# Kernel optimization log

Hardware: AMD Instinct MI355X
Metric: run time of the kernel (lower is better)

The kernel has to match this reference:

```python
import jax, jax.numpy as jnp
import numpy as np


def log_g(x):
    # log of g(x) = x + 0.5 for x>=0, sigmoid(x) for x<0
    return jnp.where(x >= 0, jnp.log(jax.nn.relu(x) + 0.5), -jax.nn.softplus(-x))


def setup_inputs() -> dict:
    key = jax.random.key(0)
    k1, k2, k3 = jax.random.split(key, 3)
    bs, seq_len, d_in, H = 4, 4096, 1024, 1024
    scale = 1.0 / np.sqrt(d_in)  # keep pre-activations O(1) so exp() in log-space scan stays finite
    x = jax.random.normal(k1, (bs, seq_len, d_in), dtype=jnp.float32)
    h_0 = jnp.zeros((bs, 1, H), dtype=jnp.float32)
    Wz = jax.random.normal(k2, (H, d_in), dtype=jnp.float32) * scale
    bz = jnp.zeros((H,), dtype=jnp.float32)
    Wh = jax.random.normal(k3, (H, d_in), dtype=jnp.float32) * scale
    bh = jnp.zeros((H,), dtype=jnp.float32)
    return {"x": x, "h_0": h_0, "Wz": Wz, "bz": bz, "Wh": Wh, "bh": bh}


def reference(x, h_0, Wz, bz, Wh, bh):
    bs, seq_len, _ = x.shape
    # gate and candidate pre-activations (two GEMMs)
    k = jnp.einsum("bsd,hd->bsh", x, Wz) + bz          # [bs, S, H]
    log_coeff = -jax.nn.softplus(k)                     # log(1 - z)
    log_z = -jax.nn.softplus(-k)                        # log(z)
    log_tilde_h = log_g(jnp.einsum("bsd,hd->bsh", x, Wh) + bh)
    log_h_0 = log_g(h_0)                                # [bs, 1, H]
    log_value = jnp.concatenate([log_h_0, log_z + log_tilde_h], axis=1)  # [bs, S+1, H]
    # log-space parallel scan: h_t = (1-z_t) h_{t-1} + z_t h~_t
    a_star = jnp.pad(jnp.cumsum(log_coeff, axis=1), ((0, 0), (1, 0), (0, 0)))  # [bs, S+1, H]
    log_h0_plus_b_star = jax.lax.cumlogsumexp(log_value - a_star, axis=1)
    log_prefix = a_star + log_h0_plus_b_star
    return jnp.exp(log_prefix)[:, 1:]                   # [bs, S, H]
```

## Files before the change

### kernel.cpp

```cpp
#include <hip/hip_runtime.h>
#include <cstddef>
#include <cstdint>

#define BSZ   4
#define SEQ   4096
#define DIN   1024
#define HDIM  1024
#define MTOT  (BSZ * SEQ)
#define NELE  ((size_t)MTOT * HDIM)
#define NX    ((size_t)MTOT * DIN)
#define NW    ((size_t)HDIM * DIN)
#define NCH   128
#define CL    (SEQ / NCH)

#define BM 128
#define BN 64
#define BK 32

#define X4 (NX / 4)
#define W4 (NW / 4)

using bf16x8 = __attribute__((ext_vector_type(8))) __bf16;
using f32x4  = __attribute__((ext_vector_type(4))) float;

__device__ __forceinline__ float bf2f(unsigned int u16bits) {
    union { unsigned int i; float f; } v;
    v.i = u16bits << 16;
    return v.f;
}
__device__ __forceinline__ unsigned int pk2(float a, float b) {
    union { float f; unsigned int i; } ua, ub; ua.f = a; ub.f = b;
    return ((ua.i + 0x8000u) >> 16) | ((ub.i + 0x8000u) & 0xffff0000u);
}

__device__ __forceinline__ void gload16(const void* g, void* l) {
    __builtin_amdgcn_global_load_lds(
        (const __attribute__((address_space(1))) unsigned int*)g,
        (__attribute__((address_space(3))) unsigned int*)l, 16, 0, 0);
}

__global__ __launch_bounds__(256) void cvt_bf16(
    const float* __restrict__ x, const float* __restrict__ wz,
    const float* __restrict__ wh, unsigned short* __restrict__ xb,
    unsigned short* __restrict__ zb, unsigned short* __restrict__ hb)
{
    const size_t i = (size_t)blockIdx.x * 256 + threadIdx.x;
    const float4* s; uint4* d; size_t off;
    const size_t xh = X4 / 2, wh4 = W4 / 2;
    if (i < xh)            { s = (const float4*)x;  d = (uint4*)xb; off = i; }
    else if (i < xh + wh4) { s = (const float4*)wz; d = (uint4*)zb; off = i - xh; }
    else                   { s = (const float4*)wh; d = (uint4*)hb; off = i - xh - wh4; }
    const float4 v0 = s[2 * off];
    const float4 v1 = s[2 * off + 1];
    uint4 r;
    r.x = pk2(v0.x, v0.y); r.y = pk2(v0.z, v0.w);
    r.z = pk2(v1.x, v1.y); r.w = pk2(v1.z, v1.w);
    d[off] = r;
}

__global__ __launch_bounds__(256, 2) void gemm_act_mfma(
    const unsigned short* __restrict__ xb, const unsigned short* __restrict__ zb,
    const unsigned short* __restrict__ hb, const float* __restrict__ bz,
    const float* __restrict__ bh, unsigned int* __restrict__ ab,
    float* __restrict__ carryA, float* __restrict__ carryB)
{
    __shared__ unsigned short xs[BM * BK];
    __shared__ unsigned short zs[BN * BK];
    __shared__ unsigned short hs[BN * BK];

    const int tid  = threadIdx.x;
    const int wid  = tid >> 6;
    const int lane = tid & 63;
    const int lm   = lane & 15;
    const int q    = lane >> 4;
    const int wy   = wid >> 1;
    const int wx   = wid & 1;

    const int m0 = blockIdx.y * BM;
    const int n0 = blockIdx.x * BN;

    const int slr   = lane >> 2;
    const int sbyte = (lane & 3) << 4;
    const char* gx = (const char*)xb + ((size_t)(m0 + wid * 32 + slr) * DIN) * 2 + sbyte;
    const char* gz = (const char*)zb + ((size_t)(n0 + wid * 16 + slr) * DIN) * 2 + sbyte;
    const char* gh = (const char*)hb + ((size_t)(n0 + wid * 16 + slr) * DIN) * 2 + sbyte;
    char* xl = (char*)xs + wid * 2048;
    char* zl = (char*)zs + wid * 1024;
    char* hl = (char*)hs + wid * 1024;

    f32x4 acc1[4][2], acc2[4][2];
#pragma unroll
    for (int mt = 0; mt < 4; ++mt)
#pragma unroll
        for (int nt = 0; nt < 2; ++nt) {
            acc1[mt][nt] = (f32x4){0.f, 0.f, 0.f, 0.f};
            acc2[mt][nt] = (f32x4){0.f, 0.f, 0.f, 0.f};
        }

    for (int k0 = 0; k0 < DIN; k0 += BK) {
        const size_t kb = (size_t)k0 * 2;
        __syncthreads();
        gload16(gx + kb,          xl);
        gload16(gx + kb + 32768,  xl + 1024);
        gload16(gz + kb,          zl);
        gload16(gh + kb,          hl);
        __syncthreads();

        bf16x8 a[4];
#pragma unroll
        for (int mt = 0; mt < 4; ++mt)
            a[mt] = *(const bf16x8*)((const char*)xs + ((wy * 64 + mt * 16 + lm) * 64 + q * 16));
#pragma unroll
        for (int nt = 0; nt < 2; ++nt) {
            const int bo = (wx * 32 + nt * 16 + lm) * 64 + q * 16;
            const bf16x8 vz = *(const bf16x8*)((const char*)zs + bo);
            const bf16x8 vh = *(const bf16x8*)((const char*)hs + bo);
#pragma unroll
            for (int mt = 0; mt < 4; ++mt) {
                acc1[mt][nt] = __builtin_amdgcn_mfma_f32_16x16x32_bf16(a[mt], vz, acc1[mt][nt], 0, 0, 0);
                acc2[mt][nt] = __builtin_amdgcn_mfma_f32_16x16x32_bf16(a[mt], vh, acc2[mt][nt], 0, 0, 0);
            }
        }
    }

    const int bi    = m0 >> 12;
    const int cbase = ((m0 & 4095) >> 5) + wy * 2;

#pragma unroll
    for (int nt = 0; nt < 2; ++nt) {
        const int col = n0 + wx * 32 + nt * 16 + lm;
        const float bzv = bz[col];
        const float bhv = bh[col];
#pragma unroll
        for (int half = 0; half < 2; ++half) {
            float CA = 1.f, CB = 0.f;
#pragma unroll
            for (int mi = 0; mi < 2; ++mi) {
                const int mt = half * 2 + mi;
                const int row0 = m0 + wy * 64 + mt * 16 + q * 4;
                float A = 1.f, B = 0.f;
#pragma unroll
                for (int r = 0; r < 4; ++r) {
                    const float kpre = acc1[mt][nt][r] + bzv;
                    const float hpre = acc2[mt][nt][r] + bhv;
                    const float ez   = __expf(-kpre);
                    const float zv   = 1.0f / (1.0f + ez);
                    const float av   = ez * zv;
                    const float g    = (hpre >= 0.f) ? (hpre + 0.5f)
                                                     : (1.0f / (1.0f + __expf(-hpre)));
                    const float bv   = zv * g;
                    ab[(size_t)(row0 + r) * HDIM + col] = pk2(av, bv);
                    A = av * A;
                    B = fmaf(av, B, bv);
                }
                float A2 = __shfl_xor(A, 16, 64);
                float B2 = __shfl_xor(B, 16, 64);
                B = (q & 1) ? fmaf(A, B2, B) : fmaf(A2, B, B2);
                A = A * A2;
                A2 = __shfl_xor(A, 32, 64);
                B2 = __shfl_xor(B, 32, 64);
                B = (q & 2) ? fmaf(A, B2, B) : fmaf(A2, B, B2);
                A = A * A2;
                CB = fmaf(A, CB, B);
                CA = A * CA;
            }
            if (q == 0) {
                const int cseq = cbase + half;
                const size_t ci = ((size_t)(cseq * BSZ + bi)) * HDIM + col;
                carryA[ci] = CA;
                carryB[ci] = CB;
            }
        }
    }
}

__global__ __launch_bounds__(256) void scan_phaseB(
    const float* __restrict__ h0, const float* __restrict__ carryA,
    const float* __restrict__ carryB, float* __restrict__ hin)
{
    const int h  = blockIdx.x * 256 + threadIdx.x;
    const int bi = blockIdx.y;
    const float v = h0[(size_t)bi * HDIM + h];
    float hr = (v >= 0.0f) ? (v + 0.5f) : (1.0f / (1.0f + __expf(-v)));
    for (int c = 0; c < NCH; ++c) {
        const size_t ci = ((size_t)c * BSZ + bi) * HDIM + h;
        hin[ci] = hr;
        hr = fmaf(carryA[ci], hr, carryB[ci]);
    }
}

__global__ __launch_bounds__(256) void scan_phaseC(
    const unsigned int* __restrict__ ab, const float* __restrict__ hin,
    float* __restrict__ out)
{
    const int c  = blockIdx.x;
    const int bi = blockIdx.y;
    const int h  = threadIdx.x * 4;
    size_t idx = ((size_t)bi * SEQ + (size_t)c * CL) * HDIM + h;
    const size_t ci = ((size_t)c * BSZ + bi) * HDIM + h;
    float4 hr = *(const float4*)&hin[ci];
#pragma unroll 4
    for (int t = 0; t < CL; ++t) {
        const uint4 v = *(const uint4*)&ab[idx];
        hr.x = fmaf(bf2f(v.x & 0xffffu), hr.x, bf2f(v.x >> 16));
        hr.y = fmaf(bf2f(v.y & 0xffffu), hr.y, bf2f(v.y >> 16));
        hr.z = fmaf(bf2f(v.z & 0xffffu), hr.z, bf2f(v.z >> 16));
        hr.w = fmaf(bf2f(v.w & 0xffffu), hr.w, bf2f(v.w >> 16));
        *(float4*)&out[idx] = hr;
        idx += HDIM;
    }
}

extern "C" void kernel_launch(void* const* d_in, const int* in_sizes, int n_in,
                              void* d_out, int out_size, void* d_ws, size_t ws_size,
                              hipStream_t stream)
{
    const float* x  = (const float*)d_in[0];
    const float* h0 = (const float*)d_in[1];
    const float* Wz = (const float*)d_in[2];
    const float* bz = (const float*)d_in[3];
    const float* Wh = (const float*)d_in[4];
    const float* bh = (const float*)d_in[5];
    float* out = (float*)d_out;

    unsigned int*   ab  = (unsigned int*)d_ws;
    unsigned short* xbf = (unsigned short*)(ab + NELE);
    unsigned short* zbf = xbf + NX;
    unsigned short* hbf = zbf + NW;
    float* carryA = (float*)(hbf + NW);
    float* carryB = carryA + (size_t)NCH * BSZ * HDIM;
    float* hin    = carryB + (size_t)NCH * BSZ * HDIM;

    const int cvtBlocks = (int)((X4 + 2 * W4) / 2 / 256);
    cvt_bf16<<<cvtBlocks, 256, 0, stream>>>(x, Wz, Wh, xbf, zbf, hbf);

    dim3 gGrid(HDIM / BN, MTOT / BM);
    gemm_act_mfma<<<gGrid, 256, 0, stream>>>(xbf, zbf, hbf, bz, bh, ab, carryA, carryB);

    dim3 bGrid(HDIM / 256, BSZ);
    scan_phaseB<<<bGrid, 256, 0, stream>>>(h0, carryA, carryB, hin);

    dim3 cGrid(NCH, BSZ);
    scan_phaseC<<<cGrid, 256, 0, stream>>>(ab, hin, out);
}
```

Measured before the change: 253.0 us.

## Rewrite fused dual GEMM as double-buffered 256x128 tile with phased MFMA schedule

Replaces the 128x64x32 single-buffered GEMM with a 512-thread kernel using 256x128x64 tiles and double-buffered LDS. Global-to-LDS prefetch of the next K tile is split across phases that alternate with MFMA bursts, using setprio and explicit waitcnt. It also adds an XOR swizzle on LDS to avoid bank conflicts and a grid swizzle for L2 locality. The aim is to hide load latency and raise MFMA utilisation. In exchange it uses many more accumulator registers and 128 KB of LDS per block, which may limit occupancy.

```diff
diff --git a/kernel.cpp b/kernel.cpp
--- a/kernel.cpp
+++ b/kernel.cpp
@@ -13,12 +13,13 @@
 #define NCH   128
 #define CL    (SEQ / NCH)
 
-#define BM 128
-#define BN 64
-#define BK 32
-
 #define X4 (NX / 4)
 #define W4 (NW / 4)
+
+#define GBM 256
+#define GBN 128
+#define GBK 64
+#define NKT (DIN / GBK)
 
 using bf16x8 = __attribute__((ext_vector_type(8))) __bf16;
 using f32x4  = __attribute__((ext_vector_type(4))) float;
@@ -58,100 +59,175 @@
     d[off] = r;
 }
 
-__global__ __launch_bounds__(256, 2) void gemm_act_mfma(
+#define MFMA16(p)                                                              \
+    _Pragma("unroll")                                                          \
+    for (int i_ = 0; i_ < 2; ++i_) {                                           \
+        _Pragma("unroll")                                                      \
+        for (int nt_ = 0; nt_ < 2; ++nt_) {                                    \
+            accz[2*(p)+i_][nt_] = __builtin_amdgcn_mfma_f32_16x16x32_bf16(     \
+                av[i_][0], fz[nt_][0], accz[2*(p)+i_][nt_], 0, 0, 0);          \
+            acch[2*(p)+i_][nt_] = __builtin_amdgcn_mfma_f32_16x16x32_bf16(     \
+                av[i_][0], fh[nt_][0], acch[2*(p)+i_][nt_], 0, 0, 0);          \
+            accz[2*(p)+i_][nt_] = __builtin_amdgcn_mfma_f32_16x16x32_bf16(     \
+                av[i_][1], fz[nt_][1], accz[2*(p)+i_][nt_], 0, 0, 0);          \
+            acch[2*(p)+i_][nt_] = __builtin_amdgcn_mfma_f32_16x16x32_bf16(     \
+                av[i_][1], fh[nt_][1], acch[2*(p)+i_][nt_], 0, 0, 0);          \
+        }                                                                      \
+    }
+
+#define PHASE(p, STAGE)                                                        \
+    {                                                                          \
+        bf16x8 av[2][2];                                                       \
+        _Pragma("unroll")                                                      \
+        for (int i_ = 0; i_ < 2; ++i_) {                                       \
+            av[i_][0] = *(const bf16x8*)(bcc + aBase + (2*(p)+i_) * 2048 + k0o);\
+            av[i_][1] = *(const bf16x8*)(bcc + aBase + (2*(p)+i_) * 2048 + k1o);\
+        }                                                                      \
+        STAGE                                                                  \
+        __builtin_amdgcn_s_barrier();                                          \
+        asm volatile("s_waitcnt lgkmcnt(0)" ::: "memory");                     \
+        __builtin_amdgcn_sched_barrier(0);                                     \
+        __builtin_amdgcn_s_setprio(1);                                         \
+        MFMA16(p)                                                              \
+        __builtin_amdgcn_s_setprio(0);                                         \
+        __builtin_amdgcn_s_barrier();                                          \
+    }
+
+__global__ __launch_bounds__(512, 2) void gemm_act_8ph(
     const unsigned short* __restrict__ xb, const unsigned short* __restrict__ zb,
     const unsigned short* __restrict__ hb, const float* __restrict__ bz,
     const float* __restrict__ bh, unsigned int* __restrict__ ab,
     float* __restrict__ carryA, float* __restrict__ carryB)
 {
-    __shared__ unsigned short xs[BM * BK];
-    __shared__ unsigned short zs[BN * BK];
-    __shared__ unsigned short hs[BN * BK];
+    __shared__ unsigned short smem[2][32768];
 
     const int tid  = threadIdx.x;
     const int wid  = tid >> 6;
     const int lane = tid & 63;
     const int lm   = lane & 15;
     const int q    = lane >> 4;
-    const int wy   = wid >> 1;
-    const int wx   = wid & 1;
-
-    const int m0 = blockIdx.y * BM;
-    const int n0 = blockIdx.x * BN;
-
-    const int slr   = lane >> 2;
-    const int sbyte = (lane & 3) << 4;
-    const char* gx = (const char*)xb + ((size_t)(m0 + wid * 32 + slr) * DIN) * 2 + sbyte;
-    const char* gz = (const char*)zb + ((size_t)(n0 + wid * 16 + slr) * DIN) * 2 + sbyte;
-    const char* gh = (const char*)hb + ((size_t)(n0 + wid * 16 + slr) * DIN) * 2 + sbyte;
-    char* xl = (char*)xs + wid * 2048;
-    char* zl = (char*)zs + wid * 1024;
-    char* hl = (char*)hs + wid * 1024;
-
-    f32x4 acc1[4][2], acc2[4][2];
-#pragma unroll
-    for (int mt = 0; mt < 4; ++mt)
+    const int wr   = wid >> 2;
+    const int wc   = wid & 3;
+
+    const int bid = blockIdx.x;
+    const int swz = (bid & 7) * 64 + (bid >> 3);
+    const int ty  = swz >> 3;
+    const int tx  = swz & 7;
+    const int m0  = ty * GBM;
+    const int n0  = tx * GBN;
+
+    const int l8   = lane >> 3;
+    const int sl   = lane & 7;
+    const int scol = 16 * (sl ^ l8);
+    const char* gA = (const char*)xb + ((size_t)(m0 + wid * 32 + l8) * DIN) * 2 + scol;
+    const char* gZ = (const char*)zb + ((size_t)(n0 + wid * 16 + l8) * DIN) * 2 + scol;
+    const char* gH = (const char*)hb + ((size_t)(n0 + wid * 16 + l8) * DIN) * 2 + scol;
+    const int ldsA = wid * 2048;
+    const int ldsZ = 16384 + wid * 1024;
+    const int ldsH = 24576 + wid * 1024;
+
+    const int sw  = (lm & 7) << 4;
+    const int k0o = (q * 16) ^ sw;
+    const int k1o = (64 + q * 16) ^ sw;
+    const int aBase = (wr * 128 + lm) * 128;
+    const int zBase = 32768 + (wc * 32 + lm) * 128;
+    const int hBase = 49152 + (wc * 32 + lm) * 128;
+
+    f32x4 accz[8][2], acch[8][2];
+#pragma unroll
+    for (int mt = 0; mt < 8; ++mt)
 #pragma unroll
         for (int nt = 0; nt < 2; ++nt) {
-            acc1[mt][nt] = (f32x4){0.f, 0.f, 0.f, 0.f};
-            acc2[mt][nt] = (f32x4){0.f, 0.f, 0.f, 0.f};
-        }
-
-    for (int k0 = 0; k0 < DIN; k0 += BK) {
-        const size_t kb = (size_t)k0 * 2;
-        __syncthreads();
-        gload16(gx + kb,          xl);
-        gload16(gx + kb + 32768,  xl + 1024);
-        gload16(gz + kb,          zl);
-        gload16(gh + kb,          hl);
-        __syncthreads();
-
-        bf16x8 a[4];
-#pragma unroll
-        for (int mt = 0; mt < 4; ++mt)
-            a[mt] = *(const bf16x8*)((const char*)xs + ((wy * 64 + mt * 16 + lm) * 64 + q * 16));
+            accz[mt][nt] = (f32x4){0.f, 0.f, 0.f, 0.f};
+            acch[mt][nt] = (f32x4){0.f, 0.f, 0.f, 0.f};
+        }
+
+    {
+        unsigned short* b0 = &smem[0][0];
+#pragma unroll
+        for (int j = 0; j < 4; ++j) gload16(gA + j * 16384, b0 + ldsA + j * 512);
+        gload16(gZ, b0 + ldsZ); gload16(gZ + 16384, b0 + ldsZ + 512);
+        gload16(gH, b0 + ldsH); gload16(gH + 16384, b0 + ldsH + 512);
+    }
+
+#pragma unroll 2
+    for (int kt = 0; kt < NKT; ++kt) {
+        const char*     bcc = (const char*)&smem[kt & 1][0];
+        unsigned short* bn  = &smem[(kt & 1) ^ 1][0];
+        const bool pf = (kt + 1 < NKT);
+        const size_t ko = (size_t)(kt + 1) * 128;
+
+        bf16x8 fz[2][2], fh[2][2];
+
+        if (pf) {
+#pragma unroll
+            for (int j = 0; j < 4; ++j)
+                gload16(gA + ko + j * 16384, bn + ldsA + j * 512);
+            asm volatile("s_waitcnt vmcnt(4)" ::: "memory");
+        } else {
+            asm volatile("s_waitcnt vmcnt(0)" ::: "memory");
+        }
+        __builtin_amdgcn_s_barrier();
 #pragma unroll
         for (int nt = 0; nt < 2; ++nt) {
-            const int bo = (wx * 32 + nt * 16 + lm) * 64 + q * 16;
-            const bf16x8 vz = *(const bf16x8*)((const char*)zs + bo);
-            const bf16x8 vh = *(const bf16x8*)((const char*)hs + bo);
-#pragma unroll
-            for (int mt = 0; mt < 4; ++mt) {
-                acc1[mt][nt] = __builtin_amdgcn_mfma_f32_16x16x32_bf16(a[mt], vz, acc1[mt][nt], 0, 0, 0);
-                acc2[mt][nt] = __builtin_amdgcn_mfma_f32_16x16x32_bf16(a[mt], vh, acc2[mt][nt], 0, 0, 0);
+            fz[nt][0] = *(const bf16x8*)(bcc + zBase + nt * 2048 + k0o);
+            fz[nt][1] = *(const bf16x8*)(bcc + zBase + nt * 2048 + k1o);
+            fh[nt][0] = *(const bf16x8*)(bcc + hBase + nt * 2048 + k0o);
+            fh[nt][1] = *(const bf16x8*)(bcc + hBase + nt * 2048 + k1o);
+        }
+        {
+            bf16x8 av[2][2];
+#pragma unroll
+            for (int i_ = 0; i_ < 2; ++i_) {
+                av[i_][0] = *(const bf16x8*)(bcc + aBase + i_ * 2048 + k0o);
+                av[i_][1] = *(const bf16x8*)(bcc + aBase + i_ * 2048 + k1o);
             }
-        }
-    }
-
-    const int bi    = m0 >> 12;
-    const int cbase = ((m0 & 4095) >> 5) + wy * 2;
+            asm volatile("s_waitcnt lgkmcnt(0)" ::: "memory");
+            __builtin_amdgcn_sched_barrier(0);
+            __builtin_amdgcn_s_setprio(1);
+            MFMA16(0)
+            __builtin_amdgcn_s_setprio(0);
+            __builtin_amdgcn_s_barrier();
+        }
+        PHASE(1,
+            if (pf) {
+                gload16(gZ + ko, bn + ldsZ); gload16(gZ + ko + 16384, bn + ldsZ + 512);
+                gload16(gH + ko, bn + ldsH); gload16(gH + ko + 16384, bn + ldsH + 512);
+            }
+        )
+        PHASE(2, )
+        PHASE(3, )
+    }
+
+    const int bi  = m0 >> 12;
+    const int cb0 = ((m0 & 4095) >> 5) + wr * 4;
 
 #pragma unroll
     for (int nt = 0; nt < 2; ++nt) {
-        const int col = n0 + wx * 32 + nt * 16 + lm;
+        const int col = n0 + wc * 32 + nt * 16 + lm;
         const float bzv = bz[col];
         const float bhv = bh[col];
 #pragma unroll
-        for (int half = 0; half < 2; ++half) {
+        for (int pr = 0; pr < 4; ++pr) {
             float CA = 1.f, CB = 0.f;
 #pragma unroll
             for (int mi = 0; mi < 2; ++mi) {
-                const int mt = half * 2 + mi;
-                const int row0 = m0 + wy * 64 + mt * 16 + q * 4;
+                const int mt   = pr * 2 + mi;
+                const int row0 = m0 + wr * 128 + mt * 16 + q * 4;
                 float A = 1.f, B = 0.f;
 #pragma unroll
                 for (int r = 0; r < 4; ++r) {
-                    const float kpre = acc1[mt][nt][r] + bzv;
-                    const float hpre = acc2[mt][nt][r] + bhv;
+                    const float kpre = accz[mt][nt][r] + bzv;
+                    const float hpre = acch[mt][nt][r] + bhv;
                     const float ez   = __expf(-kpre);
                     const float zv   = 1.0f / (1.0f + ez);
-                    const float av   = ez * zv;
+                    const float avv  = ez * zv;
                     const float g    = (hpre >= 0.f) ? (hpre + 0.5f)
                                                      : (1.0f / (1.0f + __expf(-hpre)));
                     const float bv   = zv * g;
-                    ab[(size_t)(row0 + r) * HDIM + col] = pk2(av, bv);
-                    A = av * A;
-                    B = fmaf(av, B, bv);
+                    ab[(size_t)(row0 + r) * HDIM + col] = pk2(avv, bv);
+                    A = avv * A;
+                    B = fmaf(avv, B, bv);
                 }
                 float A2 = __shfl_xor(A, 16, 64);
                 float B2 = __shfl_xor(B, 16, 64);
@@ -165,7 +241,7 @@
                 CA = A * CA;
             }
             if (q == 0) {
-                const int cseq = cbase + half;
+                const int cseq = cb0 + pr;
                 const size_t ci = ((size_t)(cseq * BSZ + bi)) * HDIM + col;
                 carryA[ci] = CA;
                 carryB[ci] = CB;
@@ -234,8 +310,8 @@
     const int cvtBlocks = (int)((X4 + 2 * W4) / 2 / 256);
     cvt_bf16<<<cvtBlocks, 256, 0, stream>>>(x, Wz, Wh, xbf, zbf, hbf);
 
-    dim3 gGrid(HDIM / BN, MTOT / BM);
-    gemm_act_mfma<<<gGrid, 256, 0, stream>>>(xbf, zbf, hbf, bz, bh, ab, carryA, carryB);
+    dim3 gGrid((MTOT / GBM) * (HDIM / GBN));
+    gemm_act_8ph<<<gGrid, 512, 0, stream>>>(xbf, zbf, hbf, bz, bh, ab, carryA, carryB);
 
     dim3 bGrid(HDIM / 256, BSZ);
     scan_phaseB<<<bGrid, 256, 0, stream>>>(h0, carryA, carryB, hin);
```

After: 241.9 us. -4.4%, faster.
